# Performance work log

Hardware: AMD Instinct MI355X
Metric: run time of the kernel (lower is better)

## Reference

```python
import jax, jax.numpy as jnp
import numpy as np
import math

H = 128
W = 128
N = 2048
DIM = 768
TWO_PI = 2.0 * math.pi
ALPHA_MIN = 1.0 / 255.0


def setup_inputs() -> dict:
    key = jax.random.key(0)
    ks = jax.random.split(key, 6)
    # _xyz = atanh(2*(rand-0.5)); clip uniform away from endpoints to avoid inf
    u = jax.random.uniform(ks[0], (N, 2), minval=1e-4, maxval=1.0 - 1e-4)
    xyz = jnp.arctanh(2.0 * (u - 0.5))
    scaling = jax.random.uniform(ks[1], (N, 2))
    rotation = jax.random.uniform(ks[2], (N, 1))
    features = jax.random.uniform(ks[3], (N, 3))
    opacity = jnp.ones((N, 1), jnp.float32)
    w_up = jax.random.normal(ks[4], (DIM, 3), jnp.float32) * 0.05
    b_up = jnp.zeros((DIM,), jnp.float32)
    x = jax.random.normal(ks[5], (1, DIM, H, W), jnp.float32)
    return {"x": x, "xyz": xyz, "scaling": scaling, "rotation": rotation,
            "features": features, "opacity": opacity, "w_up": w_up, "b_up": b_up}


def _forward(xyz, scaling, rotation, features, opacity, w_up, b_up):
    # activations (get_xyz / get_scaling / get_rotation)
    means = jnp.tanh(xyz)                                   # [N,2] in (-1,1)
    s = jnp.abs(scaling + 0.5)                              # [N,2]
    theta = jax.nn.sigmoid(rotation[:, 0]) * TWO_PI         # [N]
    c, sn = jnp.cos(theta), jnp.sin(theta)
    # M = R(theta) @ diag(s); cov2d = M M^T
    a = c * s[:, 0]; b = -sn * s[:, 1]
    d = sn * s[:, 0]; e = c * s[:, 1]
    cov_xx = a * a + b * b
    cov_xy = a * d + b * e
    cov_yy = d * d + e * e
    det = cov_xx * cov_yy - cov_xy * cov_xy
    # conic = inverse covariance (A, B, C)
    A = cov_yy / det; B = -cov_xy / det; C = cov_xx / det   # [N]
    # project [-1,1] -> pixel centers
    gx = 0.5 * (means[:, 0] + 1.0) * W                      # [N]
    gy = 0.5 * (means[:, 1] + 1.0) * H
    px = jnp.arange(W, dtype=jnp.float32) + 0.5
    py = jnp.arange(H, dtype=jnp.float32) + 0.5
    PX, PY = jnp.meshgrid(px, py)                           # [H,W], PX varies along W
    dx = gx[None, :] - PX.reshape(-1)[:, None]              # [P,N], P=H*W
    dy = gy[None, :] - PY.reshape(-1)[:, None]
    sigma = 0.5 * (A * dx * dx + C * dy * dy) + B * dx * dy # [P,N]
    alpha = jnp.minimum(0.999, opacity[:, 0][None, :] * jnp.exp(-sigma))
    alpha = jnp.where((sigma < 0.0) | (alpha < ALPHA_MIN), 0.0, alpha)
    # summation rasterizer: per-pixel weighted sum of colors
    img = jnp.clip(alpha @ features, 0.0, 1.0)              # [P,3]
    feat = img @ w_up.T + b_up                              # [P,DIM]
    return feat.T.reshape(1, DIM, H, W)


def reference(x, xyz, scaling, rotation, features, opacity, w_up, b_up):
    del x  # only its channel dim (== DIM) shapes the output in the original
    return _forward(xyz, scaling, rotation, features, opacity, w_up, b_up)
```

## Files before the change

### kernel.cpp

```cpp
#include <hip/hip_runtime.h>
#include <math.h>

#define HH 128
#define WW 128
#define NG 2048
#define DIMV 768
#define PIX (HH * WW)
#define A_MIN (1.0f / 255.0f)
#define TW 16
#define TH 4
#define NT 512
#define NWV 8
#define CH 256
#define TWO_PI 6.28318530717958647692f

__global__ __launch_bounds__(NT) void raster_kernel(
    const float* __restrict__ xyz, const float* __restrict__ scaling,
    const float* __restrict__ rotation, const float* __restrict__ features,
    const float* __restrict__ opacity, float* __restrict__ img)
{
    __shared__ int s_cnt;
    __shared__ int s_idx[NG];
    __shared__ float4 cA[CH];
    __shared__ float4 cB[CH];
    __shared__ float2 cC[CH];
    __shared__ float s_red[NWV * 64 * 3];

    int tid = threadIdx.x;
    int bx = blockIdx.x & 7, by = blockIdx.x >> 3;
    int px0 = bx * TW, py0 = by * TH;

    if (tid == 0) s_cnt = 0;
    __syncthreads();

    {
        float x0 = px0 + 0.5f, x1 = px0 + TW - 0.5f;
        float y0 = py0 + 0.5f, y1 = py0 + TH - 0.5f;
        #pragma unroll
        for (int g0 = 0; g0 < NG; g0 += NT) {
            int g = g0 + tid;
            float2 xz = ((const float2*)xyz)[g];
            float e2x = __expf(2.0f * xz.x);
            float e2y = 2.0f * __expf(2.0f * xz.y);
            float gx = (e2x / (e2x + 1.0f)) * (float)WW;
            float gy = (e2y / (e2y + 2.0f)) * (float)HH;
            float2 sc = ((const float2*)scaling)[g];
            float s0 = fabsf(sc.x + 0.5f);
            float s1 = fabsf(sc.y + 0.5f);
            float trc = s0 * s0 + s1 * s1;
            float L = __logf(255.0f * opacity[g]);
            float r2 = (L > 0.0f) ? 2.0f * L * trc * 1.0002f + 1e-3f : -1.0f;
            float ddx = fmaxf(fmaxf(x0 - gx, gx - x1), 0.0f);
            float ddy = fmaxf(fmaxf(y0 - gy, gy - y1), 0.0f);
            if (ddx * ddx + ddy * ddy <= r2) {
                int pos = atomicAdd(&s_cnt, 1);
                s_idx[pos] = g;
            }
        }
    }
    __syncthreads();
    int cnt = s_cnt;

    int lane = tid & 63, wv = tid >> 6;
    float pxf = px0 + (lane & 15) + 0.5f;
    float pyf = py0 + (lane >> 4) + 0.5f;
    float ar = 0.0f, ag = 0.0f, ab = 0.0f;

    for (int ck = 0; ck < cnt; ck += CH) {
        int csz = min(CH, cnt - ck);
        for (int j = tid; j < csz; j += NT) {
            int g = s_idx[ck + j];
            float2 xz = ((const float2*)xyz)[g];
            float e2x = __expf(2.0f * xz.x);
            float e2y = 2.0f * __expf(2.0f * xz.y);
            float gx = (e2x / (e2x + 1.0f)) * (float)WW;
            float gy = (e2y / (e2y + 2.0f)) * (float)HH;
            float2 sc = ((const float2*)scaling)[g];
            float s0 = fabsf(sc.x + 0.5f);
            float s1 = fabsf(sc.y + 0.5f);
            float th = TWO_PI / (1.0f + __expf(-rotation[g]));
            float sn = __sinf(th), cs = __cosf(th);
            float a = cs * s0, b = -sn * s1, d = sn * s0, e = cs * s1;
            float cxx = a * a + b * b;
            float cxy = a * d + b * e;
            float cyy = d * d + e * e;
            float inv = 1.0f / (cxx * cyy - cxy * cxy);
            float op = opacity[g];
            cA[j] = make_float4(0.5f * cyy * inv, -cxy * inv, 0.5f * cxx * inv, op);
            cB[j] = make_float4(gx, gy, features[3 * g + 0], features[3 * g + 1]);
            cC[j] = make_float2(features[3 * g + 2], 0.0f);
        }
        __syncthreads();
        for (int k = wv; k < csz; k += NWV) {
            float4 a0 = cA[k];
            float4 a1 = cB[k];
            float2 a2 = cC[k];
            float dx = a1.x - pxf, dy = a1.y - pyf;
            float sig = fmaf(a0.y * dx, dy, fmaf(a0.x * dx, dx, a0.z * dy * dy));
            float al = fminf(0.999f, a0.w * __expf(-sig));
            al = (sig < 0.0f || al < A_MIN) ? 0.0f : al;
            ar = fmaf(al, a1.z, ar);
            ag = fmaf(al, a1.w, ag);
            ab = fmaf(al, a2.x, ab);
        }
        __syncthreads();
    }

    s_red[(wv * 64 + lane) * 3 + 0] = ar;
    s_red[(wv * 64 + lane) * 3 + 1] = ag;
    s_red[(wv * 64 + lane) * 3 + 2] = ab;
    __syncthreads();
    if (tid < 64) {
        float sr = 0.0f, sg = 0.0f, sb = 0.0f;
        #pragma unroll
        for (int w = 0; w < NWV; ++w) {
            sr += s_red[(w * 64 + tid) * 3 + 0];
            sg += s_red[(w * 64 + tid) * 3 + 1];
            sb += s_red[(w * 64 + tid) * 3 + 2];
        }
        int p = (py0 + (tid >> 4)) * WW + px0 + (tid & 15);
        img[p]           = fminf(1.0f, fmaxf(0.0f, sr));
        img[PIX + p]     = fminf(1.0f, fmaxf(0.0f, sg));
        img[2 * PIX + p] = fminf(1.0f, fmaxf(0.0f, sb));
    }
}

__global__ __launch_bounds__(256) void project_kernel(
    const float* __restrict__ img, const float* __restrict__ w_up,
    const float* __restrict__ b_up, float* __restrict__ out)
{
    int grp = blockIdx.x >> 4;
    int seg = blockIdx.x & 15;
    int p = seg * 1024 + threadIdx.x * 4;
    float4 r = *(const float4*)(img + p);
    float4 g = *(const float4*)(img + PIX + p);
    float4 b = *(const float4*)(img + 2 * PIX + p);
    int d0 = grp * 4;
    #pragma unroll
    for (int i = 0; i < 4; ++i) {
        int d = d0 + i;
        float w0 = w_up[3 * d + 0], w1 = w_up[3 * d + 1], w2 = w_up[3 * d + 2];
        float bb = b_up[d];
        float4 v;
        v.x = fmaf(w0, r.x, fmaf(w1, g.x, fmaf(w2, b.x, bb)));
        v.y = fmaf(w0, r.y, fmaf(w1, g.y, fmaf(w2, b.y, bb)));
        v.z = fmaf(w0, r.z, fmaf(w1, g.z, fmaf(w2, b.z, bb)));
        v.w = fmaf(w0, r.w, fmaf(w1, g.w, fmaf(w2, b.w, bb)));
        *(float4*)(out + (size_t)d * PIX + p) = v;
    }
}

extern "C" void kernel_launch(void* const* d_in, const int* in_sizes, int n_in,
                              void* d_out, int out_size, void* d_ws, size_t ws_size,
                              hipStream_t stream)
{
    const float* xyz      = (const float*)d_in[1];
    const float* scaling  = (const float*)d_in[2];
    const float* rotation = (const float*)d_in[3];
    const float* features = (const float*)d_in[4];
    const float* opacity  = (const float*)d_in[5];
    const float* w_up     = (const float*)d_in[6];
    const float* b_up     = (const float*)d_in[7];
    float* out = (float*)d_out;
    float* img = (float*)d_ws;

    raster_kernel<<<256, NT, 0, stream>>>(xyz, scaling, rotation, features,
                                          opacity, img);
    project_kernel<<<(DIMV / 4) * 16, 256, 0, stream>>>(img, w_up, b_up, out);
}
```

Baseline: 109.2 us.

## Use nontemporal output stores, fast reciprocals, and vectorized image writes

```diff
diff --git a/kernel.cpp b/kernel.cpp
--- a/kernel.cpp
+++ b/kernel.cpp
@@ -14,6 +14,10 @@
 #define CH 256
 #define TWO_PI 6.28318530717958647692f
 
+typedef float v4f __attribute__((ext_vector_type(4)));
+
+__device__ __forceinline__ float frcp(float x) { return __builtin_amdgcn_rcpf(x); }
+
 __global__ __launch_bounds__(NT) void raster_kernel(
     const float* __restrict__ xyz, const float* __restrict__ scaling,
     const float* __restrict__ rotation, const float* __restrict__ features,
@@ -25,6 +29,7 @@
     __shared__ float4 cB[CH];
     __shared__ float2 cC[CH];
     __shared__ float s_red[NWV * 64 * 3];
+    __shared__ __align__(16) float s_out[3 * 64];
 
     int tid = threadIdx.x;
     int bx = blockIdx.x & 7, by = blockIdx.x >> 3;
@@ -42,8 +47,8 @@
             float2 xz = ((const float2*)xyz)[g];
             float e2x = __expf(2.0f * xz.x);
             float e2y = 2.0f * __expf(2.0f * xz.y);
-            float gx = (e2x / (e2x + 1.0f)) * (float)WW;
-            float gy = (e2y / (e2y + 2.0f)) * (float)HH;
+            float gx = e2x * frcp(e2x + 1.0f) * (float)WW;
+            float gy = e2y * frcp(e2y + 2.0f) * (float)HH;
             float2 sc = ((const float2*)scaling)[g];
             float s0 = fabsf(sc.x + 0.5f);
             float s1 = fabsf(sc.y + 0.5f);
@@ -73,18 +78,18 @@
             float2 xz = ((const float2*)xyz)[g];
             float e2x = __expf(2.0f * xz.x);
             float e2y = 2.0f * __expf(2.0f * xz.y);
-            float gx = (e2x / (e2x + 1.0f)) * (float)WW;
-            float gy = (e2y / (e2y + 2.0f)) * (float)HH;
+            float gx = e2x * frcp(e2x + 1.0f) * (float)WW;
+            float gy = e2y * frcp(e2y + 2.0f) * (float)HH;
             float2 sc = ((const float2*)scaling)[g];
             float s0 = fabsf(sc.x + 0.5f);
             float s1 = fabsf(sc.y + 0.5f);
-            float th = TWO_PI / (1.0f + __expf(-rotation[g]));
+            float th = TWO_PI * frcp(1.0f + __expf(-rotation[g]));
             float sn = __sinf(th), cs = __cosf(th);
             float a = cs * s0, b = -sn * s1, d = sn * s0, e = cs * s1;
             float cxx = a * a + b * b;
             float cxy = a * d + b * e;
             float cyy = d * d + e * e;
-            float inv = 1.0f / (cxx * cyy - cxy * cxy);
+            float inv = frcp(cxx * cyy - cxy * cxy);
             float op = opacity[g];
             cA[j] = make_float4(0.5f * cyy * inv, -cxy * inv, 0.5f * cxx * inv, op);
             cB[j] = make_float4(gx, gy, features[3 * g + 0], features[3 * g + 1]);
@@ -118,10 +123,17 @@
             sg += s_red[(w * 64 + tid) * 3 + 1];
             sb += s_red[(w * 64 + tid) * 3 + 2];
         }
-        int p = (py0 + (tid >> 4)) * WW + px0 + (tid & 15);
-        img[p]           = fminf(1.0f, fmaxf(0.0f, sr));
-        img[PIX + p]     = fminf(1.0f, fmaxf(0.0f, sg));
-        img[2 * PIX + p] = fminf(1.0f, fmaxf(0.0f, sb));
+        s_out[tid]       = fminf(1.0f, fmaxf(0.0f, sr));
+        s_out[64 + tid]  = fminf(1.0f, fmaxf(0.0f, sg));
+        s_out[128 + tid] = fminf(1.0f, fmaxf(0.0f, sb));
+    }
+    __syncthreads();
+
+    if (tid < 48) {
+        int plane = tid >> 4, q = tid & 15;
+        int row = q >> 2, c4 = q & 3;
+        float4 v = *(const float4*)&s_out[plane * 64 + row * 16 + c4 * 4];
+        *(float4*)(img + (size_t)plane * PIX + (py0 + row) * WW + px0 + c4 * 4) = v;
     }
 }
 
@@ -141,12 +153,12 @@
         int d = d0 + i;
         float w0 = w_up[3 * d + 0], w1 = w_up[3 * d + 1], w2 = w_up[3 * d + 2];
         float bb = b_up[d];
-        float4 v;
+        v4f v;
         v.x = fmaf(w0, r.x, fmaf(w1, g.x, fmaf(w2, b.x, bb)));
         v.y = fmaf(w0, r.y, fmaf(w1, g.y, fmaf(w2, b.y, bb)));
         v.z = fmaf(w0, r.z, fmaf(w1, g.z, fmaf(w2, b.z, bb)));
         v.w = fmaf(w0, r.w, fmaf(w1, g.w, fmaf(w2, b.w, bb)));
-        *(float4*)(out + (size_t)d * PIX + p) = v;
+        __builtin_nontemporal_store(v, (v4f*)(out + (size_t)d * PIX + p));
     }
 }
 
```

Result: no change. 109.6 us (+0.3%).
